# Optimization experiments

Hardware: AMD Instinct MI355X
Metric: run time of the kernel (lower is better)

## Reference

```python
import jax, jax.numpy as jnp
import numpy as np

SEQ_LEN = 720
PRED_LEN = 720
CHANNELS = 321
CUT_FREQ = 200
FREQ_OUT = 400  # int(cut_freq * (seq_len+pred_len)/seq_len)
LENGTH_RATIO = (SEQ_LEN + PRED_LEN) / SEQ_LEN  # 2.0
BATCH = 256


def setup_inputs() -> dict:
    key = jax.random.key(0)
    ks = jax.random.split(key, 8)
    scale = 1.0 / np.sqrt(CUT_FREQ)  # Linear-style init scale
    return {
        "x_enc": jax.random.normal(ks[0], (BATCH, SEQ_LEN, CHANNELS), dtype=jnp.float32),
        "x_mark_enc": jax.random.normal(ks[1], (BATCH, SEQ_LEN, 4), dtype=jnp.float32),
        "x_dec": jax.random.normal(ks[2], (BATCH, PRED_LEN, CHANNELS), dtype=jnp.float32),
        "x_mark_dec": jax.random.normal(ks[3], (BATCH, PRED_LEN, 4), dtype=jnp.float32),
        "Wr": jax.random.normal(ks[4], (CHANNELS, FREQ_OUT, CUT_FREQ), dtype=jnp.float32) * scale,
        "Wi": jax.random.normal(ks[5], (CHANNELS, FREQ_OUT, CUT_FREQ), dtype=jnp.float32) * scale,
        "br": jax.random.normal(ks[6], (CHANNELS, FREQ_OUT), dtype=jnp.float32) * scale,
        "bi": jax.random.normal(ks[7], (CHANNELS, FREQ_OUT), dtype=jnp.float32) * scale,
    }


def reference(x_enc, x_mark_enc, x_dec, x_mark_dec, Wr, Wi, br, bi):
    # RevIN-style normalization along time dim (unbiased variance, as torch.var)
    x_mean = jnp.mean(x_enc, axis=1, keepdims=True)                 # [B,1,C]
    x = x_enc - x_mean
    x_var = jnp.var(x, axis=1, keepdims=True, ddof=1)               # [B,1,C]
    x_stdev = jnp.sqrt(x_var + 1e-5)
    x = x / x_stdev

    # Low-pass in frequency domain
    x_freq = jnp.fft.rfft(x, axis=1)                                # [B, S//2+1, C] complex
    x_freq_low = x_freq[:, :CUT_FREQ, :]                            # [B, F_in, C]

    # Per-channel complex linear (the python loop over channels fused into one einsum)
    W = (Wr + 1j * Wi).astype(jnp.complex64)                        # [C, F_out, F_in]
    b = (br + 1j * bi).astype(jnp.complex64)                        # [C, F_out]
    out_freq = jnp.einsum('bfc,cof->boc', x_freq_low, W) + b.T[None]  # [B, F_out, C]

    # Back to time domain at the upsampled length
    total = SEQ_LEN + PRED_LEN
    out = jnp.fft.irfft(out_freq, n=total, axis=1) * LENGTH_RATIO   # [B, S+P, C]
    out = out[:, -PRED_LEN:, :]

    # De-normalize
    return out * x_stdev + x_mean
```

## Files before the change

### kernel.cpp

```cpp
#include <hip/hip_runtime.h>
#include <math.h>

#define SEQ    720
#define PRED   720
#define CH     321
#define FCUT   200
#define FOUT   400
#define NBATCH 256
#define NTOT   1440
#define KR     400
#define MC     800

typedef __bf16 bf16;
typedef bf16  bf16x8 __attribute__((ext_vector_type(8)));
typedef float f32x4  __attribute__((ext_vector_type(4)));

static __device__ __forceinline__ f32x4 mfma16(bf16x8 a, bf16x8 b, f32x4 c) {
    return __builtin_amdgcn_mfma_f32_16x16x32_bf16(a, b, c, 0, 0, 0);
}

__global__ void init_dmat(float* __restrict__ D) {
    int i = blockIdx.x * 256 + threadIdx.x;
    if (i >= KR * SEQ) return;
    int fp = i / SEQ, t = i % SEQ;
    int f = (fp < FCUT) ? fp : (fp - FCUT);
    int p = (f * t) % SEQ;
    float ang = (float)p * (6.28318530717958647692f / (float)SEQ);
    D[i] = (fp < FCUT) ? cosf(ang) : -sinf(ang);
}

__global__ void init_gmat(float* __restrict__ G) {
    int i = blockIdx.x * 256 + threadIdx.x;
    if (i >= SEQ * MC) return;
    int tp = i / MC, kp = i % MC;
    int t = tp + PRED;
    int k = (kp < FOUT) ? kp : (kp - FOUT);
    int p = (k * t) % NTOT;
    float ang = (float)p * (6.28318530717958647692f / (float)NTOT);
    const float s = 2.0f / (float)NTOT;
    float v;
    if (kp < FOUT) v = (k == 0) ? s : (2.0f * s * cosf(ang));
    else           v = (k == 0) ? 0.0f : (-2.0f * s * sinf(ang));
    G[i] = v;
}

__global__ void stats_kernel(const float* __restrict__ x,
                             float* __restrict__ mean_bc,
                             float* __restrict__ rstd_bc,
                             float* __restrict__ stdev_bc) {
    int i = blockIdx.x * 256 + threadIdx.x;
    if (i >= NBATCH * CH) return;
    int b = i / CH, c = i % CH;
    const float* p = x + (size_t)b * SEQ * CH + c;
    float s = 0.f, ss = 0.f;
    for (int t = 0; t < SEQ; ++t) {
        float v = p[(size_t)t * CH];
        s += v; ss += v * v;
    }
    float mean = s / (float)SEQ;
    float var = fmaxf((ss - s * mean) / (float)(SEQ - 1), 0.f);
    float st = sqrtf(var + 1e-5f);
    mean_bc[i] = mean;
    stdev_bc[i] = st;
    rstd_bc[i] = 1.0f / st;
}

template<int MODE>
__global__ __launch_bounds__(256)
void gemm_mfma(const float* __restrict__ A,
               const float* __restrict__ Bg,
               float* __restrict__ Cg,
               const float* __restrict__ P0,
               const float* __restrict__ P1,
               const float* __restrict__ P2,
               const float* __restrict__ P3,
               int Bc, int b0, int gx, int gy)
{
    const int M   = (MODE == 0) ? KR : (MODE == 1) ? MC : SEQ;
    const int K   = (MODE == 0) ? SEQ : (MODE == 1) ? KR : MC;
    const int N   = (MODE == 0) ? CH : Bc;
    const int ldb = (MODE == 0) ? CH : Bc;
    const int ldc = (MODE == 0) ? CH : Bc;

    int orig = blockIdx.x;
    int q = (int)gridDim.x >> 3, r = (int)gridDim.x & 7, xcd = orig & 7;
    int id = (xcd < r ? xcd * (q + 1) : r * (q + 1) + (xcd - r) * q) + (orig >> 3);

    const int z   = id / (gx * gy);
    const int rem = id - z * (gx * gy);
    const int my  = rem / gx;
    const int mx  = rem - my * gx;
    const int m0  = mx * 128;
    const int n0  = my * 128;

    const float* Bp = nullptr; float* Cp = nullptr;
    const float* wrc = nullptr; const float* wic = nullptr;
    const float* mnp = nullptr; const float* rsp = nullptr;
    if (MODE == 0) {
        int b = b0 + z;
        Bp  = Bg + (size_t)b * SEQ * CH;
        Cp  = Cg + (size_t)z * KR * CH;
        mnp = P0 + (size_t)b * CH;
        rsp = P1 + (size_t)b * CH;
    } else if (MODE == 1) {
        Bp  = Bg + (size_t)z * KR * Bc;
        Cp  = Cg + (size_t)z * MC * Bc;
        wrc = P0 + (size_t)z * FOUT * FCUT;
        wic = P1 + (size_t)z * FOUT * FCUT;
    } else {
        Bp  = Bg + (size_t)z * MC * Bc;
        Cp  = Cg + (size_t)z * SEQ * Bc;
    }

    __shared__ bf16 Ah[4][128][8];
    __shared__ bf16 Al[4][128][8];
    __shared__ bf16 Bh[4][128][8];
    __shared__ bf16 Bl[4][128][8];

    const int tid  = threadIdx.x;
    const int row  = tid & 127;
    const int half = tid >> 7;
    const int kloc = half * 16;

    const int lane = tid & 63;
    const int w    = tid >> 6;
    const int wm   = (w & 1) * 64;
    const int wn   = (w >> 1) * 64;
    const int fr   = lane & 15;
    const int kg   = lane >> 4;

    const int mg = m0 + row;
    const int ng = n0 + row;

    float mn = 0.f, rs = 0.f;
    if (MODE == 0 && ng < CH) { mn = mnp[ng]; rs = rsp[ng]; }

    f32x4 acc[4][4];
#pragma unroll
    for (int i = 0; i < 4; ++i)
#pragma unroll
        for (int j = 0; j < 4; ++j) acc[i][j] = (f32x4){0.f, 0.f, 0.f, 0.f};

    const int ksteps = (K + 31) / 32;
    for (int ks = 0; ks < ksteps; ++ks) {
        const int k0 = ks * 32;
        const int kb = k0 + kloc;
        const bool kval = kb < K;

        float av[16];
        if (MODE == 1) {
            if (kval && mg < M) {
                const bool hi2 = mg >= FOUT;
                const int  o   = hi2 ? mg - FOUT : mg;
#pragma unroll
                for (int qd = 0; qd < 4; ++qd) {
                    int k = kb + qd * 4;
                    bool kb2 = k >= FCUT;
                    int  k2  = kb2 ? k - FCUT : k;
                    const float* basep = (hi2 != kb2) ? wic : wrc;
                    float4 v = *(const float4*)(basep + (size_t)o * FCUT + k2);
                    float sgn = (!hi2 && kb2) ? -1.f : 1.f;
                    av[qd * 4 + 0] = sgn * v.x; av[qd * 4 + 1] = sgn * v.y;
                    av[qd * 4 + 2] = sgn * v.z; av[qd * 4 + 3] = sgn * v.w;
                }
            } else {
#pragma unroll
                for (int u = 0; u < 16; ++u) av[u] = 0.f;
            }
        } else {
            if (kval && mg < M) {
                const float* ap = A + (size_t)mg * K + kb;
#pragma unroll
                for (int qd = 0; qd < 4; ++qd) {
                    float4 v = *(const float4*)(ap + qd * 4);
                    av[qd * 4 + 0] = v.x; av[qd * 4 + 1] = v.y;
                    av[qd * 4 + 2] = v.z; av[qd * 4 + 3] = v.w;
                }
            } else {
#pragma unroll
                for (int u = 0; u < 16; ++u) av[u] = 0.f;
            }
        }

        float bv[16];
        if (kval && ng < N) {
            const float* bp = Bp + (size_t)kb * ldb + ng;
            if (MODE == 0) {
#pragma unroll
                for (int u = 0; u < 16; ++u) bv[u] = (bp[(size_t)u * ldb] - mn) * rs;
            } else {
#pragma unroll
                for (int u = 0; u < 16; ++u) bv[u] = bp[(size_t)u * ldb];
            }
        } else {
#pragma unroll
            for (int u = 0; u < 16; ++u) bv[u] = 0.f;
        }

#pragma unroll
        for (int ch = 0; ch < 2; ++ch) {
            bf16x8 ah_, al_, bh_, bl_;
#pragma unroll
            for (int e = 0; e < 8; ++e) {
                float va = av[ch * 8 + e];
                bf16 ha = (bf16)va;
                ah_[e] = ha;
                al_[e] = (bf16)(va - (float)ha);
                float vb = bv[ch * 8 + e];
                bf16 hb = (bf16)vb;
                bh_[e] = hb;
                bl_[e] = (bf16)(vb - (float)hb);
            }
            *(bf16x8*)&Ah[half * 2 + ch][row][0] = ah_;
            *(bf16x8*)&Al[half * 2 + ch][row][0] = al_;
            *(bf16x8*)&Bh[half * 2 + ch][row][0] = bh_;
            *(bf16x8*)&Bl[half * 2 + ch][row][0] = bl_;
        }
        __syncthreads();

        bf16x8 a_h[4], a_l[4];
#pragma unroll
        for (int i = 0; i < 4; ++i) {
            a_h[i] = *(const bf16x8*)&Ah[kg][wm + i * 16 + fr][0];
            a_l[i] = *(const bf16x8*)&Al[kg][wm + i * 16 + fr][0];
        }
#pragma unroll
        for (int j = 0; j < 4; ++j) {
            bf16x8 b_h = *(const bf16x8*)&Bh[kg][wn + j * 16 + fr][0];
            bf16x8 b_l = *(const bf16x8*)&Bl[kg][wn + j * 16 + fr][0];
#pragma unroll
            for (int i = 0; i < 4; ++i) {
                acc[i][j] = mfma16(a_h[i], b_h, acc[i][j]);
                acc[i][j] = mfma16(a_l[i], b_h, acc[i][j]);
                acc[i][j] = mfma16(a_h[i], b_l, acc[i][j]);
            }
        }
        __syncthreads();
    }

#pragma unroll
    for (int i = 0; i < 4; ++i) {
        const int mbase = m0 + wm + i * 16 + kg * 4;
#pragma unroll
        for (int r2 = 0; r2 < 4; ++r2) {
            const int mm = mbase + r2;
            if (mm >= M) continue;
            float bias = 0.f;
            if (MODE == 1)
                bias = (mm < FOUT) ? P2[(size_t)z * FOUT + mm]
                                   : P3[(size_t)z * FOUT + (mm - FOUT)];
#pragma unroll
            for (int j = 0; j < 4; ++j) {
                const int nn = n0 + wn + j * 16 + fr;
                if (nn < N) Cp[(size_t)mm * ldc + nn] = acc[i][j][r2] + bias;
            }
        }
    }
}

__global__ void transpose_bc(const float* __restrict__ in, float* __restrict__ out, int Bc) {
    __shared__ float tile[32][33];
    int f = blockIdx.x;
    int c0 = blockIdx.y * 32, b0 = blockIdx.z * 32;
    int tx = threadIdx.x, ty = threadIdx.y;
#pragma unroll
    for (int j = 0; j < 4; ++j) {
        int bb = b0 + ty + j * 8, cc = c0 + tx;
        if (bb < Bc && cc < CH)
            tile[ty + j * 8][tx] = in[(size_t)bb * KR * CH + (size_t)f * CH + cc];
    }
    __syncthreads();
#pragma unroll
    for (int j = 0; j < 4; ++j) {
        int cc = c0 + ty + j * 8, bb = b0 + tx;
        if (cc < CH && bb < Bc)
            out[(size_t)cc * KR * Bc + (size_t)f * Bc + bb] = tile[tx][ty + j * 8];
    }
}

__global__ void transpose_out(const float* __restrict__ outT,
                              const float* __restrict__ mean_bc,
                              const float* __restrict__ stdev_bc,
                              float* __restrict__ out, int b0, int Bc) {
    __shared__ float tile[32][33];
    int t = blockIdx.x;
    int c0 = blockIdx.y * 32, bb0 = blockIdx.z * 32;
    int tx = threadIdx.x, ty = threadIdx.y;
#pragma unroll
    for (int j = 0; j < 4; ++j) {
        int cc = c0 + ty + j * 8, bl = bb0 + tx;
        if (cc < CH && bl < Bc)
            tile[ty + j * 8][tx] = outT[(size_t)cc * SEQ * Bc + (size_t)t * Bc + bl];
    }
    __syncthreads();
#pragma unroll
    for (int j = 0; j < 4; ++j) {
        int cc = c0 + tx, bl = bb0 + ty + j * 8;
        if (cc < CH && bl < Bc) {
            int b = b0 + bl;
            size_t si = (size_t)b * CH + cc;
            out[(size_t)b * SEQ * CH + (size_t)t * CH + cc] =
                tile[tx][ty + j * 8] * stdev_bc[si] + mean_bc[si];
        }
    }
}

extern "C" void kernel_launch(void* const* d_in, const int* in_sizes, int n_in,
                              void* d_out, int out_size, void* d_ws, size_t ws_size,
                              hipStream_t stream) {
    const float* x_enc = (const float*)d_in[0];
    const float* Wr = (const float*)d_in[4];
    const float* Wi = (const float*)d_in[5];
    const float* br = (const float*)d_in[6];
    const float* bi = (const float*)d_in[7];
    float* out = (float*)d_out;

    auto al = [](size_t x) { return (x + 63) & ~(size_t)63; };
    const size_t fixedf = al((size_t)KR * SEQ) + al((size_t)SEQ * MC) + 3 * al((size_t)NBATCH * CH);

    int Bc = NBATCH;
    while (Bc > 1) {
        size_t perb = al((size_t)Bc * KR * CH) * 2 + al((size_t)Bc * MC * CH) + al((size_t)Bc * SEQ * CH);
        if ((fixedf + perb) * sizeof(float) <= ws_size) break;
        Bc >>= 1;
    }

    float* ws = (float*)d_ws;
    size_t oD = 0;
    size_t oG = oD + al((size_t)KR * SEQ);
    size_t oMean = oG + al((size_t)SEQ * MC);
    size_t oRstd = oMean + al((size_t)NBATCH * CH);
    size_t oStd = oRstd + al((size_t)NBATCH * CH);
    size_t oX = oStd + al((size_t)NBATCH * CH);
    size_t oXT = oX + al((size_t)Bc * KR * CH);
    size_t oF = oXT + al((size_t)Bc * KR * CH);
    size_t oOT = oF + al((size_t)Bc * MC * CH);

    init_dmat<<<(KR * SEQ + 255) / 256, 256, 0, stream>>>(ws + oD);
    init_gmat<<<(SEQ * MC + 255) / 256, 256, 0, stream>>>(ws + oG);
    stats_kernel<<<(NBATCH * CH + 255) / 256, 256, 0, stream>>>(x_enc, ws + oMean, ws + oRstd, ws + oStd);

    const int nch = NBATCH / Bc;
    for (int ci = 0; ci < nch; ++ci) {
        int b0 = ci * Bc;

        {
            int gx = (KR + 127) / 128, gy = (CH + 127) / 128;
            int nb = gx * gy * Bc;
            gemm_mfma<0><<<nb, 256, 0, stream>>>(ws + oD, x_enc, ws + oX,
                                                 ws + oMean, ws + oRstd, nullptr, nullptr,
                                                 Bc, b0, gx, gy);
        }

        dim3 gT1(KR, (CH + 31) / 32, (Bc + 31) / 32);
        transpose_bc<<<gT1, dim3(32, 8), 0, stream>>>(ws + oX, ws + oXT, Bc);

        {
            int gx = (MC + 127) / 128, gy = (Bc + 127) / 128;
            int nb = gx * gy * CH;
            gemm_mfma<1><<<nb, 256, 0, stream>>>(nullptr, ws + oXT, ws + oF,
                                                 Wr, Wi, br, bi,
                                                 Bc, 0, gx, gy);
        }

        {
            int gx = (SEQ + 127) / 128, gy = (Bc + 127) / 128;
            int nb = gx * gy * CH;
            gemm_mfma<2><<<nb, 256, 0, stream>>>(ws + oG, ws + oF, ws + oOT,
                                                 nullptr, nullptr, nullptr, nullptr,
                                                 Bc, 0, gx, gy);
        }

        dim3 gT3(SEQ, (CH + 31) / 32, (Bc + 31) / 32);
        transpose_out<<<gT3, dim3(32, 8), 0, stream>>>(ws + oOT, ws + oMean, ws + oStd, out, b0, Bc);
    }
}
```

Baseline: 1.908 ms.

## Switch split-precision GEMMs to fp16 with half-stored intermediates and two MFMAs

Replaces the bf16 three-MFMA hi/lo split with an fp16 scheme that splits only the A operand, keeping B as a single fp16 value. That cuts MFMA work per tile by a third and drops the B-low LDS buffer. The constant DFT matrices are now pre-split into fp16 hi/lo in global memory, so GEMMs 0 and 2 no longer convert them every k-step. Intermediates (X, XT, F) are stored as fp16 instead of fp32, which halves their memory traffic, at the cost of fp16 range and precision loss on activations.

After: 1.707 ms. 10.5% less time.

```diff
diff --git a/kernel.cpp b/kernel.cpp
--- a/kernel.cpp
+++ b/kernel.cpp
@@ -11,25 +11,31 @@
 #define KR     400
 #define MC     800
 
-typedef __bf16 bf16;
-typedef bf16  bf16x8 __attribute__((ext_vector_type(8)));
-typedef float f32x4  __attribute__((ext_vector_type(4)));
-
-static __device__ __forceinline__ f32x4 mfma16(bf16x8 a, bf16x8 b, f32x4 c) {
-    return __builtin_amdgcn_mfma_f32_16x16x32_bf16(a, b, c, 0, 0, 0);
-}
-
-__global__ void init_dmat(float* __restrict__ D) {
+typedef _Float16 f16;
+typedef f16   f16x8 __attribute__((ext_vector_type(8)));
+typedef float f32x4 __attribute__((ext_vector_type(4)));
+
+static __device__ __forceinline__ f32x4 mfma16(f16x8 a, f16x8 b, f32x4 c) {
+    return __builtin_amdgcn_mfma_f32_16x16x32_f16(a, b, c, 0, 0, 0);
+}
+static __device__ __forceinline__ f16 tof16(float v) { return (f16)v; }
+static __device__ __forceinline__ ushort f16bits(f16 h) { return __builtin_bit_cast(unsigned short, h); }
+static __device__ __forceinline__ f16 bits2f16(ushort u) { return __builtin_bit_cast(f16, u); }
+
+__global__ void init_dmat(f16* __restrict__ Dh, f16* __restrict__ Dl) {
     int i = blockIdx.x * 256 + threadIdx.x;
     if (i >= KR * SEQ) return;
     int fp = i / SEQ, t = i % SEQ;
     int f = (fp < FCUT) ? fp : (fp - FCUT);
     int p = (f * t) % SEQ;
     float ang = (float)p * (6.28318530717958647692f / (float)SEQ);
-    D[i] = (fp < FCUT) ? cosf(ang) : -sinf(ang);
-}
-
-__global__ void init_gmat(float* __restrict__ G) {
+    float v = (fp < FCUT) ? cosf(ang) : -sinf(ang);
+    f16 h = tof16(v);
+    Dh[i] = h;
+    Dl[i] = tof16(v - (float)h);
+}
+
+__global__ void init_gmat(f16* __restrict__ Gh, f16* __restrict__ Gl) {
     int i = blockIdx.x * 256 + threadIdx.x;
     if (i >= SEQ * MC) return;
     int tp = i / MC, kp = i % MC;
@@ -41,7 +47,9 @@
     float v;
     if (kp < FOUT) v = (k == 0) ? s : (2.0f * s * cosf(ang));
     else           v = (k == 0) ? 0.0f : (-2.0f * s * sinf(ang));
-    G[i] = v;
+    f16 h = tof16(v);
+    Gh[i] = h;
+    Gl[i] = tof16(v - (float)h);
 }
 
 __global__ void stats_kernel(const float* __restrict__ x,
@@ -67,9 +75,10 @@
 
 template<int MODE>
 __global__ __launch_bounds__(256)
-void gemm_mfma(const float* __restrict__ A,
-               const float* __restrict__ Bg,
-               float* __restrict__ Cg,
+void gemm_mfma(const f16* __restrict__ Ahg,
+               const f16* __restrict__ Alg,
+               const void* __restrict__ Bg,
+               void* __restrict__ Cg,
                const float* __restrict__ P0,
                const float* __restrict__ P1,
                const float* __restrict__ P2,
@@ -93,29 +102,28 @@
     const int m0  = mx * 128;
     const int n0  = my * 128;
 
-    const float* Bp = nullptr; float* Cp = nullptr;
+    const void* Bp = nullptr; void* Cp = nullptr;
     const float* wrc = nullptr; const float* wic = nullptr;
     const float* mnp = nullptr; const float* rsp = nullptr;
     if (MODE == 0) {
         int b = b0 + z;
-        Bp  = Bg + (size_t)b * SEQ * CH;
-        Cp  = Cg + (size_t)z * KR * CH;
+        Bp  = (const float*)Bg + (size_t)b * SEQ * CH;
+        Cp  = (ushort*)Cg + (size_t)z * KR * CH;
         mnp = P0 + (size_t)b * CH;
         rsp = P1 + (size_t)b * CH;
     } else if (MODE == 1) {
-        Bp  = Bg + (size_t)z * KR * Bc;
-        Cp  = Cg + (size_t)z * MC * Bc;
+        Bp  = (const ushort*)Bg + (size_t)z * KR * Bc;
+        Cp  = (ushort*)Cg + (size_t)z * MC * Bc;
         wrc = P0 + (size_t)z * FOUT * FCUT;
         wic = P1 + (size_t)z * FOUT * FCUT;
     } else {
-        Bp  = Bg + (size_t)z * MC * Bc;
-        Cp  = Cg + (size_t)z * SEQ * Bc;
-    }
-
-    __shared__ bf16 Ah[4][128][8];
-    __shared__ bf16 Al[4][128][8];
-    __shared__ bf16 Bh[4][128][8];
-    __shared__ bf16 Bl[4][128][8];
+        Bp  = (const ushort*)Bg + (size_t)z * MC * Bc;
+        Cp  = (float*)Cg + (size_t)z * SEQ * Bc;
+    }
+
+    __shared__ f16 Ah[4][128][8];
+    __shared__ f16 Al[4][128][8];
+    __shared__ f16 Bh[4][128][8];
 
     const int tid  = threadIdx.x;
     const int row  = tid & 127;
@@ -143,12 +151,11 @@
 
     const int ksteps = (K + 31) / 32;
     for (int ks = 0; ks < ksteps; ++ks) {
-        const int k0 = ks * 32;
-        const int kb = k0 + kloc;
+        const int kb = ks * 32 + kloc;
         const bool kval = kb < K;
 
-        float av[16];
         if (MODE == 1) {
+            float av[16];
             if (kval && mg < M) {
                 const bool hi2 = mg >= FOUT;
                 const int  o   = hi2 ? mg - FOUT : mg;
@@ -167,72 +174,75 @@
 #pragma unroll
                 for (int u = 0; u < 16; ++u) av[u] = 0.f;
             }
+#pragma unroll
+            for (int ch = 0; ch < 2; ++ch) {
+                f16x8 ah_, al_;
+#pragma unroll
+                for (int e = 0; e < 8; ++e) {
+                    float va = av[ch * 8 + e];
+                    f16 h = tof16(va);
+                    ah_[e] = h;
+                    al_[e] = tof16(va - (float)h);
+                }
+                *(f16x8*)&Ah[half * 2 + ch][row][0] = ah_;
+                *(f16x8*)&Al[half * 2 + ch][row][0] = al_;
+            }
         } else {
+            f16x8 h0, h1, l0, l1;
             if (kval && mg < M) {
-                const float* ap = A + (size_t)mg * K + kb;
-#pragma unroll
-                for (int qd = 0; qd < 4; ++qd) {
-                    float4 v = *(const float4*)(ap + qd * 4);
-                    av[qd * 4 + 0] = v.x; av[qd * 4 + 1] = v.y;
-                    av[qd * 4 + 2] = v.z; av[qd * 4 + 3] = v.w;
+                const f16* ph = Ahg + (size_t)mg * K + kb;
+                const f16* pl = Alg + (size_t)mg * K + kb;
+                h0 = *(const f16x8*)(ph);
+                h1 = *(const f16x8*)(ph + 8);
+                l0 = *(const f16x8*)(pl);
+                l1 = *(const f16x8*)(pl + 8);
+            } else {
+                h0 = (f16x8)(f16)0; h1 = (f16x8)(f16)0;
+                l0 = (f16x8)(f16)0; l1 = (f16x8)(f16)0;
+            }
+            *(f16x8*)&Ah[half * 2 + 0][row][0] = h0;
+            *(f16x8*)&Ah[half * 2 + 1][row][0] = h1;
+            *(f16x8*)&Al[half * 2 + 0][row][0] = l0;
+            *(f16x8*)&Al[half * 2 + 1][row][0] = l1;
+        }
+
+        {
+            f16x8 b0, b1;
+            if (kval && ng < N) {
+                if (MODE == 0) {
+                    const float* bp = (const float*)Bp + (size_t)kb * ldb + ng;
+#pragma unroll
+                    for (int u = 0; u < 8; ++u) b0[u] = tof16((bp[(size_t)u * ldb] - mn) * rs);
+#pragma unroll
+                    for (int u = 0; u < 8; ++u) b1[u] = tof16((bp[(size_t)(u + 8) * ldb] - mn) * rs);
+                } else {
+                    const ushort* bp = (const ushort*)Bp + (size_t)kb * ldb + ng;
+#pragma unroll
+                    for (int u = 0; u < 8; ++u) b0[u] = bits2f16(bp[(size_t)u * ldb]);
+#pragma unroll
+                    for (int u = 0; u < 8; ++u) b1[u] = bits2f16(bp[(size_t)(u + 8) * ldb]);
                 }
             } else {
-#pragma unroll
-                for (int u = 0; u < 16; ++u) av[u] = 0.f;
-            }
-        }
-
-        float bv[16];
-        if (kval && ng < N) {
-            const float* bp = Bp + (size_t)kb * ldb + ng;
-            if (MODE == 0) {
-#pragma unroll
-                for (int u = 0; u < 16; ++u) bv[u] = (bp[(size_t)u * ldb] - mn) * rs;
-            } else {
-#pragma unroll
-                for (int u = 0; u < 16; ++u) bv[u] = bp[(size_t)u * ldb];
-            }
-        } else {
-#pragma unroll
-            for (int u = 0; u < 16; ++u) bv[u] = 0.f;
-        }
-
-#pragma unroll
-        for (int ch = 0; ch < 2; ++ch) {
-            bf16x8 ah_, al_, bh_, bl_;
-#pragma unroll
-            for (int e = 0; e < 8; ++e) {
-                float va = av[ch * 8 + e];
-                bf16 ha = (bf16)va;
-                ah_[e] = ha;
-                al_[e] = (bf16)(va - (float)ha);
-                float vb = bv[ch * 8 + e];
-                bf16 hb = (bf16)vb;
-                bh_[e] = hb;
-                bl_[e] = (bf16)(vb - (float)hb);
-            }
-            *(bf16x8*)&Ah[half * 2 + ch][row][0] = ah_;
-            *(bf16x8*)&Al[half * 2 + ch][row][0] = al_;
-            *(bf16x8*)&Bh[half * 2 + ch][row][0] = bh_;
-            *(bf16x8*)&Bl[half * 2 + ch][row][0] = bl_;
+                b0 = (f16x8)(f16)0; b1 = (f16x8)(f16)0;
+            }
+            *(f16x8*)&Bh[half * 2 + 0][row][0] = b0;
+            *(f16x8*)&Bh[half * 2 + 1][row][0] = b1;
         }
         __syncthreads();
 
-        bf16x8 a_h[4], a_l[4];
+        f16x8 a_h[4], a_l[4];
 #pragma unroll
         for (int i = 0; i < 4; ++i) {
-            a_h[i] = *(const bf16x8*)&Ah[kg][wm + i * 16 + fr][0];
-            a_l[i] = *(const bf16x8*)&Al[kg][wm + i * 16 + fr][0];
+            a_h[i] = *(const f16x8*)&Ah[kg][wm + i * 16 + fr][0];
+            a_l[i] = *(const f16x8*)&Al[kg][wm + i * 16 + fr][0];
         }
 #pragma unroll
         for (int j = 0; j < 4; ++j) {
-            bf16x8 b_h = *(const bf16x8*)&Bh[kg][wn + j * 16 + fr][0];
-            bf16x8 b_l = *(const bf16x8*)&Bl[kg][wn + j * 16 + fr][0];
+            f16x8 b_h = *(const f16x8*)&Bh[kg][wn + j * 16 + fr][0];
 #pragma unroll
             for (int i = 0; i < 4; ++i) {
                 acc[i][j] = mfma16(a_h[i], b_h, acc[i][j]);
                 acc[i][j] = mfma16(a_l[i], b_h, acc[i][j]);
-                acc[i][j] = mfma16(a_h[i], b_l, acc[i][j]);
             }
         }
         __syncthreads();
@@ -252,14 +262,18 @@
 #pragma unroll
             for (int j = 0; j < 4; ++j) {
                 const int nn = n0 + wn + j * 16 + fr;
-                if (nn < N) Cp[(size_t)mm * ldc + nn] = acc[i][j][r2] + bias;
-            }
-        }
-    }
-}
-
-__global__ void transpose_bc(const float* __restrict__ in, float* __restrict__ out, int Bc) {
-    __shared__ float tile[32][33];
+                if (nn < N) {
+                    float v = acc[i][j][r2] + bias;
+                    if (MODE == 2) ((float*)Cp)[(size_t)mm * ldc + nn] = v;
+                    else           ((ushort*)Cp)[(size_t)mm * ldc + nn] = f16bits(tof16(v));
+                }
+            }
+        }
+    }
+}
+
+__global__ void transpose_bc(const ushort* __restrict__ in, ushort* __restrict__ out, int Bc) {
+    __shared__ ushort tile[32][34];
     int f = blockIdx.x;
     int c0 = blockIdx.y * 32, b0 = blockIdx.z * 32;
     int tx = threadIdx.x, ty = threadIdx.y;
@@ -315,30 +329,38 @@
     const float* bi = (const float*)d_in[7];
     float* out = (float*)d_out;
 
-    auto al = [](size_t x) { return (x + 63) & ~(size_t)63; };
-    const size_t fixedf = al((size_t)KR * SEQ) + al((size_t)SEQ * MC) + 3 * al((size_t)NBATCH * CH);
+    auto alb = [](size_t x) { return (x + 255) & ~(size_t)255; };
+    const size_t fixedB = 2 * alb((size_t)KR * SEQ * 2)
+                        + 2 * alb((size_t)SEQ * MC * 2)
+                        + 3 * alb((size_t)NBATCH * CH * 4);
 
     int Bc = NBATCH;
     while (Bc > 1) {
-        size_t perb = al((size_t)Bc * KR * CH) * 2 + al((size_t)Bc * MC * CH) + al((size_t)Bc * SEQ * CH);
-        if ((fixedf + perb) * sizeof(float) <= ws_size) break;
+        size_t perB = 2 * alb((size_t)Bc * KR * CH * 2)
+                    + alb((size_t)CH * MC * Bc * 2)
+                    + alb((size_t)CH * SEQ * Bc * 4);
+        if (fixedB + perB <= ws_size) break;
         Bc >>= 1;
     }
 
-    float* ws = (float*)d_ws;
-    size_t oD = 0;
-    size_t oG = oD + al((size_t)KR * SEQ);
-    size_t oMean = oG + al((size_t)SEQ * MC);
-    size_t oRstd = oMean + al((size_t)NBATCH * CH);
-    size_t oStd = oRstd + al((size_t)NBATCH * CH);
-    size_t oX = oStd + al((size_t)NBATCH * CH);
-    size_t oXT = oX + al((size_t)Bc * KR * CH);
-    size_t oF = oXT + al((size_t)Bc * KR * CH);
-    size_t oOT = oF + al((size_t)Bc * MC * CH);
-
-    init_dmat<<<(KR * SEQ + 255) / 256, 256, 0, stream>>>(ws + oD);
-    init_gmat<<<(SEQ * MC + 255) / 256, 256, 0, stream>>>(ws + oG);
-    stats_kernel<<<(NBATCH * CH + 255) / 256, 256, 0, stream>>>(x_enc, ws + oMean, ws + oRstd, ws + oStd);
+    char* wsb = (char*)d_ws;
+    size_t off = 0;
+    auto take = [&](size_t bytes) { size_t o = off; off += alb(bytes); return o; };
+    f16*    Dh   = (f16*)(wsb + take((size_t)KR * SEQ * 2));
+    f16*    Dl   = (f16*)(wsb + take((size_t)KR * SEQ * 2));
+    f16*    Gh   = (f16*)(wsb + take((size_t)SEQ * MC * 2));
+    f16*    Gl   = (f16*)(wsb + take((size_t)SEQ * MC * 2));
+    float*  Mean = (float*)(wsb + take((size_t)NBATCH * CH * 4));
+    float*  Rstd = (float*)(wsb + take((size_t)NBATCH * CH * 4));
+    float*  Stdv = (float*)(wsb + take((size_t)NBATCH * CH * 4));
+    ushort* Xb   = (ushort*)(wsb + take((size_t)Bc * KR * CH * 2));
+    ushort* XT   = (ushort*)(wsb + take((size_t)Bc * KR * CH * 2));
+    ushort* Fb   = (ushort*)(wsb + take((size_t)CH * MC * Bc * 2));
+    float*  OT   = (float*)(wsb + take((size_t)CH * SEQ * Bc * 4));
+
+    init_dmat<<<(KR * SEQ + 255) / 256, 256, 0, stream>>>(Dh, Dl);
+    init_gmat<<<(SEQ * MC + 255) / 256, 256, 0, stream>>>(Gh, Gl);
+    stats_kernel<<<(NBATCH * CH + 255) / 256, 256, 0, stream>>>(x_enc, Mean, Rstd, Stdv);
 
     const int nch = NBATCH / Bc;
     for (int ci = 0; ci < nch; ++ci) {
@@ -347,18 +369,18 @@
         {
             int gx = (KR + 127) / 128, gy = (CH + 127) / 128;
             int nb = gx * gy * Bc;
-            gemm_mfma<0><<<nb, 256, 0, stream>>>(ws + oD, x_enc, ws + oX,
-                                                 ws + oMean, ws + oRstd, nullptr, nullptr,
+            gemm_mfma<0><<<nb, 256, 0, stream>>>(Dh, Dl, (const void*)x_enc, (void*)Xb,
+                                                 Mean, Rstd, nullptr, nullptr,
                                                  Bc, b0, gx, gy);
         }
 
         dim3 gT1(KR, (CH + 31) / 32, (Bc + 31) / 32);
-        transpose_bc<<<gT1, dim3(32, 8), 0, stream>>>(ws + oX, ws + oXT, Bc);
+        transpose_bc<<<gT1, dim3(32, 8), 0, stream>>>(Xb, XT, Bc);
 
         {
             int gx = (MC + 127) / 128, gy = (Bc + 127) / 128;
             int nb = gx * gy * CH;
-            gemm_mfma<1><<<nb, 256, 0, stream>>>(nullptr, ws + oXT, ws + oF,
+            gemm_mfma<1><<<nb, 256, 0, stream>>>(nullptr, nullptr, (const void*)XT, (void*)Fb,
                                                  Wr, Wi, br, bi,
                                                  Bc, 0, gx, gy);
         }
@@ -366,12 +388,12 @@
         {
             int gx = (SEQ + 127) / 128, gy = (Bc + 127) / 128;
             int nb = gx * gy * CH;
-            gemm_mfma<2><<<nb, 256, 0, stream>>>(ws + oG, ws + oF, ws + oOT,
+            gemm_mfma<2><<<nb, 256, 0, stream>>>(Gh, Gl, (const void*)Fb, (void*)OT,
                                                  nullptr, nullptr, nullptr, nullptr,
                                                  Bc, 0, gx, gy);
         }
 
         dim3 gT3(SEQ, (CH + 31) / 32, (Bc + 31) / 32);
-        transpose_out<<<gT3, dim3(32, 8), 0, stream>>>(ws + oOT, ws + oMean, ws + oStd, out, b0, Bc);
-    }
-}
+        transpose_out<<<gT3, dim3(32, 8), 0, stream>>>(OT, Mean, Stdv, out, b0, Bc);
+    }
+}
```
